# Performance work log

Measured on AMD Instinct MI355X. Metric: run time of the kernel, lower is better.

The kernel has to match this reference:

```python
import jax, jax.numpy as jnp
import numpy as np

# dims (see shape_source): seq S = d_t+1 must equal d_k for the unary quantum loader
B, T, D_IN = 128, 127, 48
DK = 128
S = T + 1            # tokens incl. class token; S == DK
H, L = 8, 6
P = (S * S - S) // 2  # RBS angles per head (pyramid circuit over S wires)


def _pyramid_pairs(n):
    # deterministic pyramid ordering of n(n-1)/2 adjacent-pair Givens rotations
    a, b = [], []
    for k in range(n - 1):
        for i in range(k, -1, -1):
            a.append(i)
            b.append(i + 1)
    return np.asarray(a, np.int32), np.asarray(b, np.int32)


def _build_W(phi, pa, pb, n):
    # classical simulation of the RBS pyramid circuit restricted to the unary
    # subspace: product of Givens rotations -> orthogonal n x n matrix
    def step(W, inp):
        ia, ib, th = inp
        c, s = jnp.cos(th), jnp.sin(th)
        ra, rb = W[ia], W[ib]
        W = W.at[ia].set(c * ra - s * rb)
        W = W.at[ib].set(s * ra + c * rb)
        return W, None
    W0 = jnp.eye(n, dtype=phi.dtype)
    W, _ = jax.lax.scan(step, W0, (pa, pb, phi))
    return W


def _layer_norm(x, g, b, eps=1e-5):
    m = jnp.mean(x, axis=-1, keepdims=True)
    v = jnp.mean((x - m) ** 2, axis=-1, keepdims=True)
    return (x - m) * jax.lax.rsqrt(v + eps) * g + b


def setup_inputs() -> dict:
    key = jax.random.key(0)
    ks = jax.random.split(key, 8)
    f32 = jnp.float32
    return {
        "x": jax.random.normal(ks[0], (B, T, D_IN), f32),
        "embed_w": jax.random.normal(ks[1], (DK, D_IN), f32) / np.sqrt(D_IN),
        "embed_b": jnp.zeros((DK,), f32),
        "class_token": jax.random.normal(ks[2], (DK,), f32) / DK,
        "norm0_g": jnp.ones((DK,), f32),
        "norm0_b": jnp.zeros((DK,), f32),
        "Vw": jax.random.normal(ks[3], (L, H, DK, DK), f32) / np.sqrt(DK),
        "Vb": jnp.zeros((L, H, DK), f32),
        "ln_g": jnp.ones((L, H, DK), f32),
        "ln_b": jnp.zeros((L, H, DK), f32),
        "phi": jax.random.normal(ks[4], (L, H, P), f32) / np.sqrt(S),
        "merger_w": jax.random.normal(ks[5], (L, H), f32) / np.sqrt(H),
        "merger_b": jnp.zeros((L,), f32),
    }


def reference(x, embed_w, embed_b, class_token, norm0_g, norm0_b,
              Vw, Vb, ln_g, ln_b, phi, merger_w, merger_b):
    Bsz = x.shape[0]
    pa, pb = _pyramid_pairs(S)
    # orthogonal score matrices for every (layer, head)
    Ws = jax.vmap(lambda p: _build_W(p, pa, pb, S))(phi.reshape(L * H, P))
    Ws = Ws.reshape(L, H, S, S)

    # embed patches, prepend class token (pos_embedding add is a no-op in the
    # original source: bare `+self.pos_embedding` statement, so it is omitted)
    tok = jnp.einsum('btf,df->btd', x, embed_w) + embed_b
    h = jnp.concatenate([jnp.broadcast_to(class_token, (Bsz, 1, DK)), tok], axis=1)
    h = _layer_norm(h, norm0_g, norm0_b)

    scale = 1.0 / np.sqrt(DK)
    for l in range(L):
        nrm = jnp.sqrt(jnp.sum(h * h, axis=-1))      # input3: token norms [B,S]
        u = h / nrm[..., None]                        # unit tokens (convert_array)
        hh, nn, uu = h, nrm, u

        def head(W, vw, vb, g, be):
            V = jnp.einsum('bsd,ed->bse', hh, vw) + vb
            M = jnp.einsum('bsd,de,bte->bst', uu, W, uu)
            A = (M * M) * (nn[:, :, None] * nn[:, None, :])
            Pm = jax.nn.softmax(A * scale, axis=-1)
            return _layer_norm(jnp.einsum('bst,btd->bsd', Pm, V) + hh, g, be)

        hs = jax.vmap(head)(Ws[l], Vw[l], Vb[l], ln_g[l], ln_b[l])  # [H,B,S,D]
        h = jnp.einsum('hbsd,h->bsd', hs, merger_w[l]) + merger_b[l]
    return h[:, -1, :]
```

## Files before the change

kernel.cpp:

```cpp
#include <hip/hip_runtime.h>
#include <hip/hip_bf16.h>


typedef __bf16 bf16x8 __attribute__((ext_vector_type(8)));
typedef float  f32x4  __attribute__((ext_vector_type(4)));
typedef unsigned int u32;

__device__ __forceinline__ int sidx(int row, int col)
{
    return row * 128 + ((((col >> 3) ^ (row & 15)) << 3) | (col & 7));
}

__device__ __forceinline__ void gll16(const void* g, void* l)
{
    __builtin_amdgcn_global_load_lds(
        (const __attribute__((address_space(1))) void*)g,
        (__attribute__((address_space(3))) void*)l, 16, 0, 0);
}

__global__ void __launch_bounds__(256)
prep_kernel(const float* __restrict__ phi, float2* __restrict__ csn,
            const float* __restrict__ vw,  __bf16* __restrict__ cvwf)
{
    if (blockIdx.x < 3072) {
        const int mat = blockIdx.x >> 6;
        const int t   = ((blockIdx.x & 63) << 2) + (threadIdx.x >> 6);
        const int j   = threadIdx.x & 63;
        float th = 0.f;
        if (t < 253) {
            const int p = t & 1, i = 2 * j + p;
            const int lim = min(t, 252 - t);
            if (i <= lim) {
                const int k = (t + i) >> 1;
                th = phi[mat * 8128 + ((k * (k + 1)) >> 1) + (k - i)];
            }
        }
        float sn, cs;
        __sincosf(th, &sn, &cs);
        csn[(mat * 256 + t) * 64 + j] = make_float2(cs, sn);
    } else {
        const int f    = (blockIdx.x - 3072) * 256 + threadIdx.x;
        const int lane = f & 63;
        const int k0   = (f >> 6) & 3;
        const int t    = (f >> 8) & 7;
        const int lh   = f >> 11;
        const int row  = t * 16 + (lane & 15);
        const int col  = k0 * 32 + (lane >> 4) * 8;
        const float* src = vw + (lh * 128 + row) * 128 + col;
        __bf16* dst = cvwf + f * 8;
#pragma unroll
        for (int j2 = 0; j2 < 8; j2++) dst[j2] = (__bf16)src[j2];
    }
}

__global__ void __launch_bounds__(64)
build_w_kernel(const float2* __restrict__ csn, __bf16* __restrict__ wt)
{
    const int mat = blockIdx.x >> 5;
    const int grp = blockIdx.x & 31;
    const int c0  = grp * 4;
    const int lam = threadIdx.x;

    const float2* base = csn + (mat * 256) * 64 + lam;

    float vlo[4], vhi[4];
#pragma unroll
    for (int j = 0; j < 4; j++) {
        vlo[j] = (2 * lam     == c0 + j) ? 1.f : 0.f;
        vhi[j] = (2 * lam + 1 == c0 + j) ? 1.f : 0.f;
    }

    float2 buf[3][16];
#pragma unroll
    for (int k = 0; k < 16; k++) buf[0][k] = base[k * 64];
#pragma unroll
    for (int k = 0; k < 16; k++) buf[1][k] = base[(16 + k) * 64];

#pragma unroll
    for (int g = 0; g < 16; g++) {
        const int cb = g % 3;
        if (g < 14) {
            const int nb = (g + 2) % 3;
#pragma unroll
            for (int k = 0; k < 16; k++)
                buf[nb][k] = base[((g + 2) * 16 + k) * 64];
        }
#pragma unroll
        for (int p = 0; p < 8; p++) {
            {
                const float cs = buf[cb][2 * p].x, sn = buf[cb][2 * p].y;
#pragma unroll
                for (int j = 0; j < 4; j++) {
                    float lo = vlo[j], hi = vhi[j];
                    vlo[j] = cs * lo - sn * hi;
                    vhi[j] = sn * lo + cs * hi;
                }
            }
            {
                const float cs = buf[cb][2 * p + 1].x, sn = buf[cb][2 * p + 1].y;
#pragma unroll
                for (int j = 0; j < 4; j++) {
                    float y  = __shfl_down(vlo[j], 1);
                    float x  = vhi[j];
                    float xn = cs * x - sn * y;
                    float yn = sn * x + cs * y;
                    vhi[j] = xn;
                    float z = __shfl_up(yn, 1);
                    if (lam > 0) vlo[j] = z;
                }
            }
        }
    }

    const int t    = c0 >> 4;
    const int k0w  = lam >> 4;
    const int quad = (lam >> 2) & 3;
    u32* wtu = (u32*)wt;
#pragma unroll
    for (int j = 0; j < 4; j++) {
        __bf16 va = (__bf16)vlo[j];
        __bf16 vb = (__bf16)vhi[j];
        u32 pk = (u32)__builtin_bit_cast(unsigned short, va)
               | ((u32)__builtin_bit_cast(unsigned short, vb) << 16);
        const int frag = (t * 4 + k0w) * 64 + quad * 16 + ((c0 & 15) + j);
        wtu[mat * 8192 + frag * 4 + (lam & 3)] = pk;
    }
}

__global__ void __launch_bounds__(512)
embed_kernel(const float* __restrict__ x,  const float* __restrict__ ew,
             const float* __restrict__ eb, const float* __restrict__ ct,
             const float* __restrict__ g0, const float* __restrict__ b0,
             float* __restrict__ hf, __bf16* __restrict__ hb,
             float* __restrict__ invn)
{
    __shared__ float sx[4][48];
    __shared__ float sred[4][2];
    const int d  = threadIdx.x & 127, sq = threadIdx.x >> 7;
    const int wh = (threadIdx.x >> 6) & 1;
    const int b  = blockIdx.x & 127;
    const int s  = (blockIdx.x >> 7) * 4 + sq;

    if (s > 0 && d < 48) sx[sq][d] = x[(b * 127 + (s - 1)) * 48 + d];
    __syncthreads();

    float val;
    if (s == 0) {
        val = ct[d];
    } else {
        float aa = 0.f;
#pragma unroll
        for (int f = 0; f < 48; f++) aa = fmaf(sx[sq][f], ew[d * 48 + f], aa);
        val = aa + eb[d];
    }
    float v = val;
#pragma unroll
    for (int m = 32; m; m >>= 1) v += __shfl_xor(v, m);
    if ((threadIdx.x & 63) == 0) sred[sq][wh] = v;
    __syncthreads();
    float mean = (sred[sq][0] + sred[sq][1]) * (1.f / 128.f);
    float xc   = val - mean;
    __syncthreads();
    v = xc * xc;
#pragma unroll
    for (int m = 32; m; m >>= 1) v += __shfl_xor(v, m);
    if ((threadIdx.x & 63) == 0) sred[sq][wh] = v;
    __syncthreads();
    float var = (sred[sq][0] + sred[sq][1]) * (1.f / 128.f);
    float y   = xc * rsqrtf(var + 1e-5f) * g0[d] + b0[d];
    __syncthreads();
    v = y * y;
#pragma unroll
    for (int m = 32; m; m >>= 1) v += __shfl_xor(v, m);
    if ((threadIdx.x & 63) == 0) sred[sq][wh] = v;
    __syncthreads();
    float ss = sred[sq][0] + sred[sq][1];

    const int o = (b * 128 + s) * 128 + d;
    hf[o] = y;
    hb[o] = (__bf16)y;
    if (d == 0) invn[b * 128 + s] = rsqrtf(ss);
}

__global__ void __launch_bounds__(512, 4)
attn_kernel(int l, int last,
            const float*  __restrict__ hf,  const __bf16* __restrict__ hb,
            const float*  __restrict__ invn, const __bf16* __restrict__ wt,
            const __bf16* __restrict__ vwf, const float* __restrict__ vb,
            const float* __restrict__ lng,  const float* __restrict__ lnb,
            const float* __restrict__ mwp,  __bf16* __restrict__ hs)
{
    __shared__ __align__(16) __bf16 sH[128 * 128];
    __shared__ __align__(16) __bf16 sY[128 * 128];
    __shared__ float sInv[128];
    __shared__ float sVb[128];
    __shared__ float sLg[128];
    __shared__ float sLb[128];

    const int tid  = threadIdx.x;
    const int lane = tid & 63, w = tid >> 6;
    const int l15  = lane & 15, quad = lane >> 4;
    const int b    = blockIdx.x & 127;
    const int hh   = blockIdx.x >> 7;
    const int lh   = l * 8 + hh;

    const __bf16* hbp   = hb  + b * 16384;
    const __bf16* wbase = wt  + (size_t)lh * 16384;
    const __bf16* vbase = vwf + (size_t)lh * 16384;

#pragma unroll
    for (int c = 0; c < 4; c++) {
        const int ch  = tid + c * 512;
        const int row = ch >> 4, cc = ch & 15;
        const int sc  = cc ^ (row & 15);
        gll16(hbp + (row * 16 + sc) * 8, &sH[(c * 512 + w * 64) * 8]);
    }
    if (tid < 128) {
        sInv[tid] = invn[b * 128 + tid];
        sVb[tid]  = vb[lh * 128 + tid];
        sLg[tid]  = lng[lh * 128 + tid];
        sLb[tid]  = lnb[lh * 128 + tid];
    }
    __syncthreads();

    const int r0 = w * 16;
    const int kq = quad * 8;
    const int q4 = quad * 4;
    const f32x4 vzero = {0.f, 0.f, 0.f, 0.f};
    const bool active = !last || (w == 7);

    f32x4 acc[8];

    auto mmL = [&](const __bf16* Ab, const __bf16* Bb) {
#pragma unroll
        for (int t = 0; t < 8; t++) acc[t] = vzero;
        __builtin_amdgcn_s_setprio(1);
#pragma unroll
        for (int k0 = 0; k0 < 128; k0 += 32) {
            const int kk = k0 + kq;
            bf16x8 a0 = *(const bf16x8*)(&Ab[sidx(r0 + l15, kk)]);
#pragma unroll
            for (int t = 0; t < 8; t++) {
                bf16x8 bb = *(const bf16x8*)(&Bb[sidx(t * 16 + l15, kk)]);
                acc[t] = __builtin_amdgcn_mfma_f32_16x16x32_bf16(a0, bb, acc[t], 0, 0, 0);
            }
        }
        __builtin_amdgcn_s_setprio(0);
    };

    auto mmG = [&](const __bf16* gB) {
#pragma unroll
        for (int t = 0; t < 8; t++) acc[t] = vzero;
        __builtin_amdgcn_s_setprio(1);
#pragma unroll
        for (int k0c = 0; k0c < 4; k0c++) {
            const int kk = k0c * 32 + kq;
            bf16x8 a0 = *(const bf16x8*)(&sH[sidx(r0 + l15, kk)]);
#pragma unroll
            for (int t = 0; t < 8; t++) {
                bf16x8 bb = *(const bf16x8*)(gB + ((t * 4 + k0c) * 64 + lane) * 8);
                acc[t] = __builtin_amdgcn_mfma_f32_16x16x32_bf16(a0, bb, acc[t], 0, 0, 0);
            }
        }
        __builtin_amdgcn_s_setprio(0);
    };

    float hres[8][4];

    if (active) {
        mmG(wbase);
#pragma unroll
        for (int t = 0; t < 8; t++)
#pragma unroll
            for (int r = 0; r < 4; r++)
                sY[sidx(r0 + q4 + r, t * 16 + l15)] = (__bf16)acc[t][r];

        mmL(sY, sH);

        {
            const float scale2 = 0.08838834764831843f * 1.4426950408889634f;
            float invt[8];
#pragma unroll
            for (int t = 0; t < 8; t++) invt[t] = sInv[t * 16 + l15];
            float invs[4];
#pragma unroll
            for (int r = 0; r < 4; r++) invs[r] = sInv[r0 + q4 + r];

            float mx[4] = {-3e38f, -3e38f, -3e38f, -3e38f};
#pragma unroll
            for (int t = 0; t < 8; t++)
#pragma unroll
                for (int r = 0; r < 4; r++) {
                    float g = acc[t][r];
                    float v = g * g * invs[r] * invt[t] * scale2;
                    acc[t][r] = v;
                    mx[r] = fmaxf(mx[r], v);
                }
#pragma unroll
            for (int m = 1; m < 16; m <<= 1)
#pragma unroll
                for (int r = 0; r < 4; r++) mx[r] = fmaxf(mx[r], __shfl_xor(mx[r], m));

            float sm[4] = {0.f, 0.f, 0.f, 0.f};
#pragma unroll
            for (int t = 0; t < 8; t++)
#pragma unroll
                for (int r = 0; r < 4; r++) {
                    float e = exp2f(acc[t][r] - mx[r]);
                    acc[t][r] = e;
                    sm[r] += e;
                }
#pragma unroll
            for (int m = 1; m < 16; m <<= 1)
#pragma unroll
                for (int r = 0; r < 4; r++) sm[r] += __shfl_xor(sm[r], m);
#pragma unroll
            for (int r = 0; r < 4; r++) sm[r] = 1.0f / sm[r];
#pragma unroll
            for (int t = 0; t < 8; t++)
#pragma unroll
                for (int r = 0; r < 4; r++)
                    sY[sidx(r0 + q4 + r, t * 16 + l15)] = (__bf16)(acc[t][r] * sm[r]);
        }

        {
            const float* hfp = hf + (b * 128 + r0 + q4) * 128;
#pragma unroll
            for (int t = 0; t < 8; t++)
#pragma unroll
                for (int r = 0; r < 4; r++)
                    hres[t][r] = hfp[r * 128 + t * 16 + l15];
        }
    }

    mmG(vbase);
    __syncthreads();

    {
        float vbv[8];
#pragma unroll
        for (int t = 0; t < 8; t++) vbv[t] = sVb[t * 16 + l15];
#pragma unroll
        for (int t = 0; t < 8; t++)
#pragma unroll
            for (int r = 0; r < 4; r++)
                sH[sidx(t * 16 + l15, r0 + q4 + r)] = (__bf16)(acc[t][r] + vbv[t]);
    }
    __syncthreads();

    if (active) {
        mmL(sY, sH);

        {
            const float mw = mwp[lh];
            float lgv[8], lbv[8];
#pragma unroll
            for (int t = 0; t < 8; t++) {
                lgv[t] = sLg[t * 16 + l15];
                lbv[t] = sLb[t * 16 + l15];
            }
            float sum_[4] = {0.f, 0.f, 0.f, 0.f};
            float sq_[4]  = {0.f, 0.f, 0.f, 0.f};
#pragma unroll
            for (int t = 0; t < 8; t++)
#pragma unroll
                for (int r = 0; r < 4; r++) {
                    float xx = acc[t][r] + hres[t][r];
                    acc[t][r] = xx;
                    sum_[r] += xx;
                    sq_[r]  += xx * xx;
                }
#pragma unroll
            for (int m = 1; m < 16; m <<= 1)
#pragma unroll
                for (int r = 0; r < 4; r++) {
                    sum_[r] += __shfl_xor(sum_[r], m);
                    sq_[r]  += __shfl_xor(sq_[r], m);
                }
            float mean[4], rstd[4];
#pragma unroll
            for (int r = 0; r < 4; r++) {
                mean[r] = sum_[r] * (1.f / 128.f);
                float var = sq_[r] * (1.f / 128.f) - mean[r] * mean[r];
                rstd[r] = rsqrtf(fmaxf(var, 0.f) + 1e-5f);
            }
            __bf16* hsp = hs + ((hh * 128 + b) * 128 + r0 + q4) * 128;
#pragma unroll
            for (int t = 0; t < 8; t++)
#pragma unroll
                for (int r = 0; r < 4; r++) {
                    if (!last || (q4 + r == 15)) {
                        float y = (acc[t][r] - mean[r]) * rstd[r] * lgv[t] + lbv[t];
                        hsp[r * 128 + t * 16 + l15] = (__bf16)(y * mw);
                    }
                }
        }
    }
}

__global__ void __launch_bounds__(256)
merge_kernel(const __bf16* __restrict__ hs, const float* __restrict__ mbp, int l,
             float* __restrict__ hf, __bf16* __restrict__ hb, float* __restrict__ invn,
             float* __restrict__ out, int last)
{
    const int ln = threadIdx.x & 63;
    const int d2 = ln * 2;
    const float mbv = mbp[l];

    int b, s;
    if (last) {
        b = blockIdx.x * 4 + (threadIdx.x >> 6);
        s = 127;
    } else {
        b = blockIdx.x & 127;
        s = (blockIdx.x >> 7) * 4 + (threadIdx.x >> 6);
    }

    float a0 = mbv, a1 = mbv;
#pragma unroll
    for (int h8 = 0; h8 < 8; h8++) {
        const __bf16* p = hs + (((size_t)h8 * 128 + b) * 128 + s) * 128 + d2;
        a0 += (float)p[0];
        a1 += (float)p[1];
    }

    if (last) {
        *(float2*)(out + b * 128 + d2) = make_float2(a0, a1);
        return;
    }

    float v = a0 * a0 + a1 * a1;
#pragma unroll
    for (int m = 32; m; m >>= 1) v += __shfl_xor(v, m);

    const size_t o = ((size_t)b * 128 + s) * 128 + d2;
    *(float2*)(hf + o) = make_float2(a0, a1);
    __bf16 p0 = (__bf16)a0, p1 = (__bf16)a1;
    ((u32*)hb)[o >> 1] = (u32)__builtin_bit_cast(unsigned short, p0)
                       | ((u32)__builtin_bit_cast(unsigned short, p1) << 16);
    if (ln == 0) invn[b * 128 + s] = rsqrtf(v);
}

extern "C" void kernel_launch(void* const* d_in, const int* in_sizes, int n_in,
                              void* d_out, int out_size, void* d_ws, size_t ws_size,
                              hipStream_t stream)
{
    (void)in_sizes; (void)n_in; (void)out_size; (void)ws_size;

    const float* x   = (const float*)d_in[0];
    const float* ew  = (const float*)d_in[1];
    const float* eb  = (const float*)d_in[2];
    const float* ct  = (const float*)d_in[3];
    const float* g0  = (const float*)d_in[4];
    const float* b0  = (const float*)d_in[5];
    const float* vw  = (const float*)d_in[6];
    const float* vb  = (const float*)d_in[7];
    const float* lng = (const float*)d_in[8];
    const float* lnb = (const float*)d_in[9];
    const float* phi = (const float*)d_in[10];
    const float* mw  = (const float*)d_in[11];
    const float* mb  = (const float*)d_in[12];
    float* out = (float*)d_out;

    char* ws = (char*)d_ws;
    __bf16* wt   = (__bf16*)(ws);
    float*  hf   = (float*)(ws + 1572864);
    __bf16* hb   = (__bf16*)(ws + 9961472);
    float*  invn = (float*)(ws + 14155776);
    __bf16* hs   = (__bf16*)(ws + 14221312);
    __bf16* cvwf = (__bf16*)(ws + 47775744);
    float2* csn  = (float2*)(ws + 49348608);

    prep_kernel<<<3456, 256, 0, stream>>>(phi, csn, vw, cvwf);
    build_w_kernel<<<1536, 64, 0, stream>>>(csn, wt);
    embed_kernel<<<4096, 512, 0, stream>>>(x, ew, eb, ct, g0, b0, hf, hb, invn);
    for (int l = 0; l < 6; l++) {
        const int last = (l == 5) ? 1 : 0;
        attn_kernel<<<1024, 512, 0, stream>>>(l, last, hf, hb, invn, wt, cvwf,
                                              vb, lng, lnb, mw, hs);
        merge_kernel<<<last ? 32 : 4096, 256, 0, stream>>>(hs, mb, l, hf, hb,
                                                           invn, out, last);
    }
}
```

Baseline: 388.5 us.

## Store activations in MFMA fragment layout and read operands directly from global

Embed and merge kernels now write the bf16 activations in a pre-swizzled MFMA fragment order. The attention kernel then loads its A and B operands straight from global/L2 instead of staging the hidden-state tile in LDS. The V projection is computed transposed (Vw as A, h as B) into a new sV buffer. Small per-row parameters (inverse norms, bias, layernorm gamma and beta) are read directly from global instead of through shared memory. This removes the LDS staging and one barrier, and frees shared memory for occupancy, at the cost of more redundant global/L2 reads of the activation tile across waves.

```diff
diff --git a/kernel.cpp b/kernel.cpp
--- a/kernel.cpp
+++ b/kernel.cpp
@@ -9,13 +9,6 @@
 __device__ __forceinline__ int sidx(int row, int col)
 {
     return row * 128 + ((((col >> 3) ^ (row & 15)) << 3) | (col & 7));
-}
-
-__device__ __forceinline__ void gll16(const void* g, void* l)
-{
-    __builtin_amdgcn_global_load_lds(
-        (const __attribute__((address_space(1))) void*)g,
-        (__attribute__((address_space(3))) void*)l, 16, 0, 0);
 }
 
 __global__ void __launch_bounds__(256)
@@ -131,7 +124,7 @@
 embed_kernel(const float* __restrict__ x,  const float* __restrict__ ew,
              const float* __restrict__ eb, const float* __restrict__ ct,
              const float* __restrict__ g0, const float* __restrict__ b0,
-             float* __restrict__ hf, __bf16* __restrict__ hb,
+             float* __restrict__ hf, __bf16* __restrict__ hbf,
              float* __restrict__ invn)
 {
     __shared__ float sx[4][48];
@@ -176,26 +169,23 @@
     __syncthreads();
     float ss = sred[sq][0] + sred[sq][1];
 
-    const int o = (b * 128 + s) * 128 + d;
-    hf[o] = y;
-    hb[o] = (__bf16)y;
+    hf[(b * 128 + s) * 128 + d] = y;
+    const int fr  = (s >> 4) * 4 + (d >> 5);
+    const int ln2 = (s & 15) | (((d >> 3) & 3) << 4);
+    hbf[b * 16384 + fr * 512 + ln2 * 8 + (d & 7)] = (__bf16)y;
     if (d == 0) invn[b * 128 + s] = rsqrtf(ss);
 }
 
 __global__ void __launch_bounds__(512, 4)
 attn_kernel(int l, int last,
-            const float*  __restrict__ hf,  const __bf16* __restrict__ hb,
+            const float*  __restrict__ hf,  const __bf16* __restrict__ hbf,
             const float*  __restrict__ invn, const __bf16* __restrict__ wt,
             const __bf16* __restrict__ vwf, const float* __restrict__ vb,
             const float* __restrict__ lng,  const float* __restrict__ lnb,
             const float* __restrict__ mwp,  __bf16* __restrict__ hs)
 {
-    __shared__ __align__(16) __bf16 sH[128 * 128];
     __shared__ __align__(16) __bf16 sY[128 * 128];
-    __shared__ float sInv[128];
-    __shared__ float sVb[128];
-    __shared__ float sLg[128];
-    __shared__ float sLb[128];
+    __shared__ __align__(16) __bf16 sV[128 * 128];
 
     const int tid  = threadIdx.x;
     const int lane = tid & 63, w = tid >> 6;
@@ -204,24 +194,9 @@
     const int hh   = blockIdx.x >> 7;
     const int lh   = l * 8 + hh;
 
-    const __bf16* hbp   = hb  + b * 16384;
+    const __bf16* hfb   = hbf + (size_t)b  * 16384;
     const __bf16* wbase = wt  + (size_t)lh * 16384;
     const __bf16* vbase = vwf + (size_t)lh * 16384;
-
-#pragma unroll
-    for (int c = 0; c < 4; c++) {
-        const int ch  = tid + c * 512;
-        const int row = ch >> 4, cc = ch & 15;
-        const int sc  = cc ^ (row & 15);
-        gll16(hbp + (row * 16 + sc) * 8, &sH[(c * 512 + w * 64) * 8]);
-    }
-    if (tid < 128) {
-        sInv[tid] = invn[b * 128 + tid];
-        sVb[tid]  = vb[lh * 128 + tid];
-        sLg[tid]  = lng[lh * 128 + tid];
-        sLb[tid]  = lnb[lh * 128 + tid];
-    }
-    __syncthreads();
 
     const int r0 = w * 16;
     const int kq = quad * 8;
@@ -230,8 +205,40 @@
     const bool active = !last || (w == 7);
 
     f32x4 acc[8];
-
-    auto mmL = [&](const __bf16* Ab, const __bf16* Bb) {
+    float hres[8][4];
+
+    auto mmRG = [&](const bf16x8* A4, const __bf16* gB) {
+#pragma unroll
+        for (int t = 0; t < 8; t++) acc[t] = vzero;
+        __builtin_amdgcn_s_setprio(1);
+#pragma unroll
+        for (int k0c = 0; k0c < 4; k0c++) {
+#pragma unroll
+            for (int t = 0; t < 8; t++) {
+                bf16x8 bb = *(const bf16x8*)(gB + ((t * 4 + k0c) * 64 + lane) * 8);
+                acc[t] = __builtin_amdgcn_mfma_f32_16x16x32_bf16(A4[k0c], bb, acc[t], 0, 0, 0);
+            }
+        }
+        __builtin_amdgcn_s_setprio(0);
+    };
+
+    auto mmLG = [&](const __bf16* Ab, const __bf16* gB) {
+#pragma unroll
+        for (int t = 0; t < 8; t++) acc[t] = vzero;
+        __builtin_amdgcn_s_setprio(1);
+#pragma unroll
+        for (int k0c = 0; k0c < 4; k0c++) {
+            bf16x8 a0 = *(const bf16x8*)(&Ab[sidx(r0 + l15, k0c * 32 + kq)]);
+#pragma unroll
+            for (int t = 0; t < 8; t++) {
+                bf16x8 bb = *(const bf16x8*)(gB + ((t * 4 + k0c) * 64 + lane) * 8);
+                acc[t] = __builtin_amdgcn_mfma_f32_16x16x32_bf16(a0, bb, acc[t], 0, 0, 0);
+            }
+        }
+        __builtin_amdgcn_s_setprio(0);
+    };
+
+    auto mmLL = [&](const __bf16* Ab, const __bf16* Bb) {
 #pragma unroll
         for (int t = 0; t < 8; t++) acc[t] = vzero;
         __builtin_amdgcn_s_setprio(1);
@@ -248,43 +255,28 @@
         __builtin_amdgcn_s_setprio(0);
     };
 
-    auto mmG = [&](const __bf16* gB) {
-#pragma unroll
-        for (int t = 0; t < 8; t++) acc[t] = vzero;
-        __builtin_amdgcn_s_setprio(1);
-#pragma unroll
-        for (int k0c = 0; k0c < 4; k0c++) {
-            const int kk = k0c * 32 + kq;
-            bf16x8 a0 = *(const bf16x8*)(&sH[sidx(r0 + l15, kk)]);
-#pragma unroll
-            for (int t = 0; t < 8; t++) {
-                bf16x8 bb = *(const bf16x8*)(gB + ((t * 4 + k0c) * 64 + lane) * 8);
-                acc[t] = __builtin_amdgcn_mfma_f32_16x16x32_bf16(a0, bb, acc[t], 0, 0, 0);
-            }
-        }
-        __builtin_amdgcn_s_setprio(0);
-    };
-
-    float hres[8][4];
-
     if (active) {
-        mmG(wbase);
+        bf16x8 ha[4];
+#pragma unroll
+        for (int k0 = 0; k0 < 4; k0++)
+            ha[k0] = *(const bf16x8*)(hfb + ((w * 4 + k0) * 64 + lane) * 8);
+        mmRG(ha, wbase);
 #pragma unroll
         for (int t = 0; t < 8; t++)
 #pragma unroll
             for (int r = 0; r < 4; r++)
                 sY[sidx(r0 + q4 + r, t * 16 + l15)] = (__bf16)acc[t][r];
 
-        mmL(sY, sH);
+        mmLG(sY, hfb);
 
         {
             const float scale2 = 0.08838834764831843f * 1.4426950408889634f;
             float invt[8];
 #pragma unroll
-            for (int t = 0; t < 8; t++) invt[t] = sInv[t * 16 + l15];
+            for (int t = 0; t < 8; t++) invt[t] = invn[b * 128 + t * 16 + l15];
             float invs[4];
 #pragma unroll
-            for (int r = 0; r < 4; r++) invs[r] = sInv[r0 + q4 + r];
+            for (int r = 0; r < 4; r++) invs[r] = invn[b * 128 + r0 + q4 + r];
 
             float mx[4] = {-3e38f, -3e38f, -3e38f, -3e38f};
 #pragma unroll
@@ -333,31 +325,34 @@
         }
     }
 
-    mmG(vbase);
-    __syncthreads();
-
     {
-        float vbv[8];
-#pragma unroll
-        for (int t = 0; t < 8; t++) vbv[t] = sVb[t * 16 + l15];
+        bf16x8 va[4];
+#pragma unroll
+        for (int k0 = 0; k0 < 4; k0++)
+            va[k0] = *(const bf16x8*)(vbase + ((w * 4 + k0) * 64 + lane) * 8);
+        mmRG(va, hfb);
+
+        float vbr[4];
+#pragma unroll
+        for (int r = 0; r < 4; r++) vbr[r] = vb[lh * 128 + r0 + q4 + r];
 #pragma unroll
         for (int t = 0; t < 8; t++)
 #pragma unroll
             for (int r = 0; r < 4; r++)
-                sH[sidx(t * 16 + l15, r0 + q4 + r)] = (__bf16)(acc[t][r] + vbv[t]);
+                sV[sidx(r0 + q4 + r, t * 16 + l15)] = (__bf16)(acc[t][r] + vbr[r]);
     }
     __syncthreads();
 
     if (active) {
-        mmL(sY, sH);
+        mmLL(sY, sV);
 
         {
             const float mw = mwp[lh];
             float lgv[8], lbv[8];
 #pragma unroll
             for (int t = 0; t < 8; t++) {
-                lgv[t] = sLg[t * 16 + l15];
-                lbv[t] = sLb[t * 16 + l15];
+                lgv[t] = lng[lh * 128 + t * 16 + l15];
+                lbv[t] = lnb[lh * 128 + t * 16 + l15];
             }
             float sum_[4] = {0.f, 0.f, 0.f, 0.f};
             float sq_[4]  = {0.f, 0.f, 0.f, 0.f};
@@ -400,7 +395,7 @@
 
 __global__ void __launch_bounds__(256)
 merge_kernel(const __bf16* __restrict__ hs, const float* __restrict__ mbp, int l,
-             float* __restrict__ hf, __bf16* __restrict__ hb, float* __restrict__ invn,
+             float* __restrict__ hf, __bf16* __restrict__ hbf, float* __restrict__ invn,
              float* __restrict__ out, int last)
 {
     const int ln = threadIdx.x & 63;
@@ -435,9 +430,15 @@
 
     const size_t o = ((size_t)b * 128 + s) * 128 + d2;
     *(float2*)(hf + o) = make_float2(a0, a1);
+
     __bf16 p0 = (__bf16)a0, p1 = (__bf16)a1;
-    ((u32*)hb)[o >> 1] = (u32)__builtin_bit_cast(unsigned short, p0)
-                       | ((u32)__builtin_bit_cast(unsigned short, p1) << 16);
+    u32 pk = (u32)__builtin_bit_cast(unsigned short, p0)
+           | ((u32)__builtin_bit_cast(unsigned short, p1) << 16);
+    const int fr  = (s >> 4) * 4 + (ln >> 4);
+    const int ln2 = (s & 15) | (((ln >> 2) & 3) << 4);
+    const size_t oh = (size_t)b * 16384 + fr * 512 + ln2 * 8 + (ln & 3) * 2;
+    *(u32*)(hbf + oh) = pk;
+
     if (ln == 0) invn[b * 128 + s] = rsqrtf(v);
 }
 
@@ -465,7 +466,7 @@
     char* ws = (char*)d_ws;
     __bf16* wt   = (__bf16*)(ws);
     float*  hf   = (float*)(ws + 1572864);
-    __bf16* hb   = (__bf16*)(ws + 9961472);
+    __bf16* hbf  = (__bf16*)(ws + 9961472);
     float*  invn = (float*)(ws + 14155776);
     __bf16* hs   = (__bf16*)(ws + 14221312);
     __bf16* cvwf = (__bf16*)(ws + 47775744);
@@ -473,12 +474,12 @@
 
     prep_kernel<<<3456, 256, 0, stream>>>(phi, csn, vw, cvwf);
     build_w_kernel<<<1536, 64, 0, stream>>>(csn, wt);
-    embed_kernel<<<4096, 512, 0, stream>>>(x, ew, eb, ct, g0, b0, hf, hb, invn);
+    embed_kernel<<<4096, 512, 0, stream>>>(x, ew, eb, ct, g0, b0, hf, hbf, invn);
     for (int l = 0; l < 6; l++) {
         const int last = (l == 5) ? 1 : 0;
-        attn_kernel<<<1024, 512, 0, stream>>>(l, last, hf, hb, invn, wt, cvwf,
+        attn_kernel<<<1024, 512, 0, stream>>>(l, last, hf, hbf, invn, wt, cvwf,
                                               vb, lng, lnb, mw, hs);
-        merge_kernel<<<last ? 32 : 4096, 256, 0, stream>>>(hs, mb, l, hf, hb,
+        merge_kernel<<<last ? 32 : 4096, 256, 0, stream>>>(hs, mb, l, hf, hbf,
                                                            invn, out, last);
     }
 }
```

Result: slower. 617.7 us (+59.0%).
